# Kernel optimization log

Measured on AMD Instinct MI355X. Metric: run time of the kernel, lower is better.

Reference implementation:

```python
import jax, jax.numpy as jnp
import numpy as np
from jax import lax

S, B, VIN, VOUT, U, E = 64, 256, 128, 128, 1024, 512
START_CODE = 0
T_DEC = 25  # MAX_DECODE_STEPS


def gru_step(x, h, Wih, Whh, bih, bhh):
    # PyTorch GRU cell, gate order r,z,n
    gi = x @ Wih.T + bih
    gh = h @ Whh.T + bhh
    ir, iz, inn = jnp.split(gi, 3, axis=-1)
    hr, hz, hn = jnp.split(gh, 3, axis=-1)
    r = jax.nn.sigmoid(ir + hr)
    z = jax.nn.sigmoid(iz + hz)
    n = jnp.tanh(inn + r * hn)
    return (1.0 - z) * n + z * h


def setup_inputs() -> dict:
    key = jax.random.key(0)
    ks = jax.random.split(key, 20)
    sc = 0.05
    inp = {
        'x': jax.random.normal(ks[0], (S, B, VIN), jnp.float32),
        'x_len': jnp.maximum(jnp.sort(jax.random.randint(ks[1], (B,), 0, S + 1)), 1),
        'enc_Wih': jax.random.normal(ks[2], (3 * U, VIN), jnp.float32) * sc,
        'enc_Whh': jax.random.normal(ks[3], (3 * U, U), jnp.float32) * sc,
        'enc_bih': jnp.zeros((3 * U,), jnp.float32),
        'enc_bhh': jnp.zeros((3 * U,), jnp.float32),
        'dec_Wih': jax.random.normal(ks[4], (3 * U, E + U), jnp.float32) * sc,
        'dec_Whh': jax.random.normal(ks[5], (3 * U, U), jnp.float32) * sc,
        'dec_bih': jnp.zeros((3 * U,), jnp.float32),
        'dec_bhh': jnp.zeros((3 * U,), jnp.float32),
        'o2h_W': jax.random.normal(ks[6], (E, VOUT), jnp.float32) * sc,
        'o2h_b': jnp.zeros((E,), jnp.float32),
        'fc_W': jax.random.normal(ks[7], (VOUT, U), jnp.float32) * sc,
        'fc_b': jnp.zeros((VOUT,), jnp.float32),
        'W1_W': jax.random.normal(ks[8], (U, U), jnp.float32) * sc,
        'W1_b': jnp.zeros((U,), jnp.float32),
        'W2_W': jax.random.normal(ks[9], (U, U), jnp.float32) * sc,
        'W2_b': jnp.zeros((U,), jnp.float32),
        'V_W': jax.random.normal(ks[10], (1, U), jnp.float32) * sc,
        'V_b': jnp.zeros((1,), jnp.float32),
    }
    return inp


def _forward(x, x_len, enc_Wih, enc_Whh, enc_bih, enc_bhh,
             dec_Wih, dec_Whh, dec_bih, dec_bhh,
             o2h_W, o2h_b, fc_W, fc_b, W1_W, W1_b, W2_W, W2_b, V_W, V_b):
    # ---- Encoder GRU with length masking (pack/pad semantics) ----
    h0 = jnp.zeros((B, U), jnp.float32)
    t_idx = jnp.arange(S)

    def enc_step(h, inp_t):
        xt, t = inp_t
        mask = (t < x_len)[:, None]  # [B,1]
        hn = gru_step(xt, h, enc_Wih, enc_Whh, enc_bih, enc_bhh)
        h = jnp.where(mask, hn, h)
        out = jnp.where(mask, hn, 0.0)
        return h, out

    enc_hidden, enc_out = lax.scan(enc_step, h0, (x, t_idx))  # enc_out [S,B,U]
    enc_out = jnp.transpose(enc_out, (1, 0, 2))  # [B,S,U]

    # ---- Greedy decode (teacher_force=False), 25 steps ----
    enc_proj = enc_out @ W1_W.T + W1_b  # precompute W1(enc_output), [B,S,U]
    start = jnp.zeros((B, VOUT), jnp.float32).at[:, START_CODE].set(1.0)

    def dec_step(carry, _):
        h, dec_in = carry
        score = jnp.tanh(enc_proj + (h @ W2_W.T + W2_b)[:, None, :])  # [B,S,U]
        logits = score @ V_W.T + V_b  # [B,S,1]
        attn = jax.nn.softmax(logits, axis=1)
        ctx = jnp.sum(attn * enc_out, axis=1)  # [B,U]
        emb = dec_in @ o2h_W.T + o2h_b  # [B,E]
        gx = jnp.concatenate([ctx, emb], axis=-1)
        hn = gru_step(gx, h, dec_Wih, dec_Whh, dec_bih, dec_bhh)
        pred = hn @ fc_W.T + fc_b  # [B,VOUT]
        onehot = jax.nn.one_hot(jnp.argmax(pred, axis=-1), VOUT, dtype=pred.dtype)
        return (hn, lax.stop_gradient(onehot)), pred

    _, preds = lax.scan(dec_step, (enc_hidden, start), None, length=T_DEC - 1)
    return jnp.concatenate([start[None], preds], axis=0)  # [25,B,VOUT]


def reference(x, x_len, enc_Wih, enc_Whh, enc_bih, enc_bhh,
              dec_Wih, dec_Whh, dec_bih, dec_bhh,
              o2h_W, o2h_b, fc_W, fc_b, W1_W, W1_b, W2_W, W2_b, V_W, V_b):
    return _forward(x, x_len, enc_Wih, enc_Whh, enc_bih, enc_bhh,
                    dec_Wih, dec_Whh, dec_bih, dec_bhh,
                    o2h_W, o2h_b, fc_W, fc_b, W1_W, W1_b, W2_W, W2_b, V_W, V_b)
```

## Files before the change

### kernel.cpp

```cpp
#include <hip/hip_runtime.h>
#include <math.h>

#define SLEN 64
#define BATCH 256
#define VIND 128
#define VOUTD 128
#define UDIM 1024
#define EDIM 512
#define TDEC 25
#define GXW 1536
#define U3 3072
#define NSEG 12

typedef __attribute__((ext_vector_type(8))) short short8;
typedef __attribute__((ext_vector_type(4))) float f32x4;

#define MFMA(acc, A, B) acc = __builtin_amdgcn_mfma_f32_16x16x32_bf16((A), (B), (acc), 0, 0, 0)

__device__ __forceinline__ float sigm(float x) { return 1.f / (1.f + expf(-x)); }

__device__ __forceinline__ float tanhf_fast(float x) {
    float ax = fabsf(x);
    float e = __expf(-2.f * ax);
    float t = (1.f - e) / (1.f + e);
    return copysignf(t, x);
}

__device__ __forceinline__ short f2bf(float f) {
    unsigned u = __float_as_uint(f);
    u += 0x7FFF + ((u >> 16) & 1);
    return (short)(u >> 16);
}
__device__ __forceinline__ float bf2f(short h) {
    return __uint_as_float(((unsigned)(unsigned short)h) << 16);
}

__device__ __forceinline__ size_t pkChunk(int r, int k, int K) {
    return ((size_t)(r >> 4) * (K >> 5) + (k >> 5)) * 64 + ((r & 15) + 16 * ((k >> 3) & 3));
}

union S8 { short s[8]; short8 v; };

__device__ __forceinline__ void writeSplit8(short* Hi, short* Lo, size_t chunk,
                                            const float* vals) {
    S8 h, l;
#pragma unroll
    for (int j = 0; j < 8; j++) {
        short hb = f2bf(vals[j]);
        h.s[j] = hb;
        l.s[j] = f2bf(vals[j] - bf2f(hb));
    }
    ((short8*)Hi)[chunk] = h.v;
    ((short8*)Lo)[chunk] = l.v;
}

__global__ void init_kernel(float* __restrict__ h0, short* __restrict__ hpHi,
                            short* __restrict__ hpLo, float* __restrict__ out0,
                            int* __restrict__ idx,
                            const float* __restrict__ o2h_W,
                            const float* __restrict__ o2h_b,
                            float* __restrict__ o2hT) {
    int i = blockIdx.x * 256 + threadIdx.x;
    if (i < BATCH * UDIM) { h0[i] = 0.f; hpHi[i] = 0; hpLo[i] = 0; }
    if (i < BATCH * VOUTD) out0[i] = ((i & (VOUTD - 1)) == 0) ? 1.f : 0.f;
    if (i < BATCH) idx[i] = 0;
    if (i < VOUTD * EDIM) {
        int v = i >> 9, e = i & (EDIM - 1);
        o2hT[i] = o2h_W[(size_t)e * VOUTD + v] + o2h_b[e];
    }
}

struct PackSeg {
    const float* sA; const float* sB;
    short* Hi; short* Lo;
    int KA, KB, offA, offB, chunkStart;
};
struct PackArgs { PackSeg s[NSEG]; };

__global__ void pack_all(PackArgs pa, int total) {
    int gid = blockIdx.x * 256 + threadIdx.x;
    if (gid >= total) return;
    int si = 0;
#pragma unroll
    for (int i = 1; i < NSEG; i++) si = (gid >= pa.s[i].chunkStart) ? i : si;
    PackSeg sg = pa.s[si];
    int local = gid - sg.chunkStart;
    int K = sg.KA + sg.KB;
    int cpr = K >> 3;
    int r = local / cpr, k0 = (local - r * cpr) * 8;
    const float* src = (k0 < sg.KA)
        ? sg.sA + (size_t)(sg.offA + r) * sg.KA + k0
        : sg.sB + (size_t)(sg.offB + r) * sg.KB + (k0 - sg.KA);
    float v[8];
#pragma unroll
    for (int j = 0; j < 8; j++) v[j] = src[j];
    writeSplit8(sg.Hi, sg.Lo, pkChunk(r, k0, K), v);
}

__global__ __launch_bounds__(256) void gemm_w(
    const short8* __restrict__ Ahi, const short8* __restrict__ Alo,
    const short8* __restrict__ Whi, const short8* __restrict__ Wlo,
    const float* __restrict__ bias, float* __restrict__ C,
    int KT, int N) {
    int tid = threadIdx.x, lane = tid & 63, wave = tid >> 6;
    int m16 = blockIdx.x * 4 + (wave & 1) * 2;
    int nb = blockIdx.y * 8 + (wave >> 1) * 4;
    const short8* a0h = Ahi + (size_t)m16 * KT * 64 + lane;
    const short8* a1h = a0h + (size_t)KT * 64;
    const short8* a0l = Alo + (size_t)m16 * KT * 64 + lane;
    const short8* a1l = a0l + (size_t)KT * 64;
    const short8* w0h = Whi + (size_t)(nb + 0) * KT * 64 + lane;
    const short8* w1h = Whi + (size_t)(nb + 1) * KT * 64 + lane;
    const short8* w2h = Whi + (size_t)(nb + 2) * KT * 64 + lane;
    const short8* w3h = Whi + (size_t)(nb + 3) * KT * 64 + lane;
    const short8* w0l = Wlo + (size_t)(nb + 0) * KT * 64 + lane;
    const short8* w1l = Wlo + (size_t)(nb + 1) * KT * 64 + lane;
    const short8* w2l = Wlo + (size_t)(nb + 2) * KT * 64 + lane;
    const short8* w3l = Wlo + (size_t)(nb + 3) * KT * 64 + lane;
    f32x4 acc0[4] = {}, acc1[4] = {};

    for (int kt = 0; kt < KT; kt++) {
        size_t o = (size_t)kt * 64;
        short8 A0H = a0h[o], A1H = a1h[o], A0L = a0l[o], A1L = a1l[o];
        short8 WH0 = w0h[o], WL0 = w0l[o];
        MFMA(acc0[0], A0H, WH0); MFMA(acc1[0], A1H, WH0);
        MFMA(acc0[0], A0H, WL0); MFMA(acc1[0], A1H, WL0);
        MFMA(acc0[0], A0L, WH0); MFMA(acc1[0], A1L, WH0);
        short8 WH1 = w1h[o], WL1 = w1l[o];
        MFMA(acc0[1], A0H, WH1); MFMA(acc1[1], A1H, WH1);
        MFMA(acc0[1], A0H, WL1); MFMA(acc1[1], A1H, WL1);
        MFMA(acc0[1], A0L, WH1); MFMA(acc1[1], A1L, WH1);
        short8 WH2 = w2h[o], WL2 = w2l[o];
        MFMA(acc0[2], A0H, WH2); MFMA(acc1[2], A1H, WH2);
        MFMA(acc0[2], A0H, WL2); MFMA(acc1[2], A1H, WL2);
        MFMA(acc0[2], A0L, WH2); MFMA(acc1[2], A1L, WH2);
        short8 WH3 = w3h[o], WL3 = w3l[o];
        MFMA(acc0[3], A0H, WH3); MFMA(acc1[3], A1H, WH3);
        MFMA(acc0[3], A0H, WL3); MFMA(acc1[3], A1H, WL3);
        MFMA(acc0[3], A0L, WH3); MFMA(acc1[3], A1L, WH3);
    }
    int rsub = (lane >> 4) * 4, cn = lane & 15;
    int row0 = (m16 + 0) * 16 + rsub;
    int row1 = (m16 + 1) * 16 + rsub;
#pragma unroll
    for (int j = 0; j < 4; j++) {
        int col = (nb + j) * 16 + cn;
        float bb = bias ? bias[col] : 0.f;
#pragma unroll
        for (int r = 0; r < 4; r++) {
            C[(size_t)(row0 + r) * N + col] = acc0[j][r] + bb;
            C[(size_t)(row1 + r) * N + col] = acc1[j][r] + bb;
        }
    }
}

__global__ __launch_bounds__(256) void gemm_bm32(
    const short8* __restrict__ Ahi, const short8* __restrict__ Alo,
    const short8* __restrict__ Whi, const short8* __restrict__ Wlo,
    const float* __restrict__ bias, float* __restrict__ C,
    int KT, int N) {
    int tid = threadIdx.x, lane = tid & 63, wave = tid >> 6;
    int m16 = blockIdx.x * 2 + (wave & 1);
    int n16 = blockIdx.y * 4 + (wave >> 1) * 2;
    const short8* ah = Ahi + (size_t)m16 * KT * 64 + lane;
    const short8* al = Alo + (size_t)m16 * KT * 64 + lane;
    const short8* w0h = Whi + (size_t)n16 * KT * 64 + lane;
    const short8* w1h = w0h + (size_t)KT * 64;
    const short8* w0l = Wlo + (size_t)n16 * KT * 64 + lane;
    const short8* w1l = w0l + (size_t)KT * 64;
    f32x4 a0 = {0,0,0,0}, a1 = {0,0,0,0};
    for (int kt = 0; kt < KT; kt++) {
        size_t o = (size_t)kt * 64;
        short8 AH = ah[o], AL = al[o];
        short8 W0H = w0h[o], W0L = w0l[o], W1H = w1h[o], W1L = w1l[o];
        MFMA(a0, AH, W0H); MFMA(a1, AH, W1H);
        MFMA(a0, AH, W0L); MFMA(a1, AH, W1L);
        MFMA(a0, AL, W0H); MFMA(a1, AL, W1H);
    }
    int rsub = (lane >> 4) * 4, cn = lane & 15;
    float b0 = bias ? bias[(n16 + 0) * 16 + cn] : 0.f;
    float b1 = bias ? bias[(n16 + 1) * 16 + cn] : 0.f;
#pragma unroll
    for (int r = 0; r < 4; r++) {
        int row = m16 * 16 + rsub + r;
        C[(size_t)row * N + (n16 + 0) * 16 + cn] = a0[r] + b0;
        C[(size_t)row * N + (n16 + 1) * 16 + cn] = a1[r] + b1;
    }
}

__global__ __launch_bounds__(384) void enc_gru3(
    const short8* __restrict__ hinH8, const short8* __restrict__ hinL8,
    const short8* __restrict__ WrH, const short8* __restrict__ WrL,
    const short8* __restrict__ WzH, const short8* __restrict__ WzL,
    const short8* __restrict__ WnH, const short8* __restrict__ WnL,
    const float* __restrict__ gi,
    const float* __restrict__ bih, const float* __restrict__ bhh,
    const float* __restrict__ hinF, float* __restrict__ houtF,
    short* __restrict__ hoH, short* __restrict__ hoL,
    short* __restrict__ eaHi, short* __restrict__ eaLo,
    const int* __restrict__ x_len, int t) {
    __shared__ float sC[6][16][16];
    __shared__ float sHo[16][16];
    __shared__ float sEo[16][16];
    int tid = threadIdx.x, lane = tid & 63, wave = tid >> 6;
    int g = blockIdx.x;
    int m16 = blockIdx.y;
    int gate = wave >> 1, half = wave & 1;
    const short8* ah = hinH8 + (size_t)m16 * 32 * 64 + (size_t)half * 16 * 64 + lane;
    const short8* al = hinL8 + (size_t)m16 * 32 * 64 + (size_t)half * 16 * 64 + lane;
    const short8* WH0 = (gate == 0) ? WrH : (gate == 1) ? WzH : WnH;
    const short8* WL0 = (gate == 0) ? WrL : (gate == 1) ? WzL : WnL;
    const short8* wh = WH0 + (size_t)g * 32 * 64 + (size_t)half * 16 * 64 + lane;
    const short8* wl = WL0 + (size_t)g * 32 * 64 + (size_t)half * 16 * 64 + lane;
    f32x4 acc = {0, 0, 0, 0};
    for (int kt = 0; kt < 16; kt++) {
        size_t o = (size_t)kt * 64;
        short8 AH = ah[o], AL = al[o];
        short8 WH = wh[o], WL = wl[o];
        MFMA(acc, AH, WH);
        MFMA(acc, AH, WL);
        MFMA(acc, AL, WH);
    }
    {
        int rsub = (lane >> 4) << 2, cn = lane & 15;
#pragma unroll
        for (int j = 0; j < 4; j++) sC[wave][rsub + j][cn] = acc[j];
    }
    __syncthreads();
    if (wave == 0) {
        int cu = g * 16 + (lane & 15);
        int rsub = (lane >> 4) << 2;
        float b_r = bih[cu] + bhh[cu];
        float b_z = bih[UDIM + cu] + bhh[UDIM + cu];
        float b_nh = bhh[2 * UDIM + cu];
        float b_ni = bih[2 * UDIM + cu];
        int growLocal = (t & 7) * 256;
#pragma unroll
        for (int j = 0; j < 4; j++) {
            int rr = rsub + j, cc = lane & 15;
            int b = m16 * 16 + rr;
            const float* gr = gi + (size_t)(growLocal + b) * U3;
            float rg = sigm(sC[0][rr][cc] + sC[1][rr][cc] + gr[cu] + b_r);
            float zg = sigm(sC[2][rr][cc] + sC[3][rr][cc] + gr[UDIM + cu] + b_z);
            float nn = tanhf(gr[2 * UDIM + cu] + b_ni +
                             rg * (sC[4][rr][cc] + sC[5][rr][cc] + b_nh));
            float hp = hinF[(size_t)b * UDIM + cu];
            float hv = (1.f - zg) * nn + zg * hp;
            bool msk = t < x_len[b];
            float ho = msk ? hv : hp;
            houtF[(size_t)b * UDIM + cu] = ho;
            sHo[rr][cc] = ho;
            sEo[rr][cc] = msk ? hv : 0.f;
        }
    }
    __syncthreads();
    if (wave == 1 && lane < 32) {
        int rr = lane >> 1, oct = lane & 1;
        int brow = m16 * 16 + rr;
        int u0 = g * 16 + oct * 8;
        float v[8];
#pragma unroll
        for (int j = 0; j < 8; j++) v[j] = sHo[rr][oct * 8 + j];
        writeSplit8(hoH, hoL, pkChunk(brow, u0, UDIM), v);
#pragma unroll
        for (int j = 0; j < 8; j++) v[j] = sEo[rr][oct * 8 + j];
        writeSplit8(eaHi, eaLo, pkChunk(brow * SLEN + t, u0, UDIM), v);
    }
}

__global__ __launch_bounds__(384) void dec_gru3(
    const short8* __restrict__ hinH8, const short8* __restrict__ hinL8,
    const short8* __restrict__ gxH8, const short8* __restrict__ gxL8,
    const short8* __restrict__ WrH, const short8* __restrict__ WrL,
    const short8* __restrict__ WzH, const short8* __restrict__ WzL,
    const short8* __restrict__ WnhH, const short8* __restrict__ WnhL,
    const short8* __restrict__ WniH, const short8* __restrict__ WniL,
    const float* __restrict__ bih, const float* __restrict__ bhh,
    const float* __restrict__ hinF, float* __restrict__ houtF,
    short* __restrict__ hoH, short* __restrict__ hoL) {
    __shared__ float sC[8][16][16];
    __shared__ float sHo[16][16];
    int tid = threadIdx.x, lane = tid & 63, wave = tid >> 6;
    int g = blockIdx.x;
    int m16 = blockIdx.y;
    int gate = wave >> 1, half = wave & 1;
    const short8* ah = hinH8 + (size_t)m16 * 32 * 64 + (size_t)half * 16 * 64 + lane;
    const short8* al = hinL8 + (size_t)m16 * 32 * 64 + (size_t)half * 16 * 64 + lane;
    const short8* gxh = gxH8 + (size_t)m16 * 48 * 64 + (size_t)half * 24 * 64 + lane;
    const short8* gxl = gxL8 + (size_t)m16 * 48 * 64 + (size_t)half * 24 * 64 + lane;
    const short8 *whA, *wlA, *whB, *wlB;
    if (gate == 0) {
        whA = WrH + (size_t)g * 80 * 64 + (size_t)half * 16 * 64 + lane;
        wlA = WrL + (size_t)g * 80 * 64 + (size_t)half * 16 * 64 + lane;
        whB = WrH + (size_t)g * 80 * 64 + (size_t)(32 + half * 24) * 64 + lane;
        wlB = WrL + (size_t)g * 80 * 64 + (size_t)(32 + half * 24) * 64 + lane;
    } else if (gate == 1) {
        whA = WzH + (size_t)g * 80 * 64 + (size_t)half * 16 * 64 + lane;
        wlA = WzL + (size_t)g * 80 * 64 + (size_t)half * 16 * 64 + lane;
        whB = WzH + (size_t)g * 80 * 64 + (size_t)(32 + half * 24) * 64 + lane;
        wlB = WzL + (size_t)g * 80 * 64 + (size_t)(32 + half * 24) * 64 + lane;
    } else {
        whA = WnhH + (size_t)g * 32 * 64 + (size_t)half * 16 * 64 + lane;
        wlA = WnhL + (size_t)g * 32 * 64 + (size_t)half * 16 * 64 + lane;
        whB = WniH + (size_t)g * 48 * 64 + (size_t)half * 24 * 64 + lane;
        wlB = WniL + (size_t)g * 48 * 64 + (size_t)half * 24 * 64 + lane;
    }
    f32x4 accA = {0,0,0,0}, accB = {0,0,0,0};
    for (int kt = 0; kt < 16; kt++) {
        size_t o = (size_t)kt * 64;
        short8 AH = ah[o], AL = al[o];
        short8 WH = whA[o], WL = wlA[o];
        MFMA(accA, AH, WH);
        MFMA(accA, AH, WL);
        MFMA(accA, AL, WH);
    }
    for (int kt = 0; kt < 24; kt++) {
        size_t o = (size_t)kt * 64;
        short8 AH = gxh[o], AL = gxl[o];
        short8 WH = whB[o], WL = wlB[o];
        MFMA(accB, AH, WH);
        MFMA(accB, AH, WL);
        MFMA(accB, AL, WH);
    }
    {
        int rsub = (lane >> 4) << 2, cn = lane & 15;
        if (wave < 4) {
#pragma unroll
            for (int j = 0; j < 4; j++) sC[wave][rsub + j][cn] = accA[j] + accB[j];
        } else {
#pragma unroll
            for (int j = 0; j < 4; j++) {
                sC[wave][rsub + j][cn] = accA[j];
                sC[wave + 2][rsub + j][cn] = accB[j];
            }
        }
    }
    __syncthreads();
    if (wave == 0) {
        int cu = g * 16 + (lane & 15);
        int rsub = (lane >> 4) << 2;
        float b_r = bih[cu] + bhh[cu];
        float b_z = bih[UDIM + cu] + bhh[UDIM + cu];
        float b_nh = bhh[2 * UDIM + cu];
        float b_ni = bih[2 * UDIM + cu];
#pragma unroll
        for (int j = 0; j < 4; j++) {
            int rr = rsub + j, cc = lane & 15;
            int b = m16 * 16 + rr;
            float rg = sigm(sC[0][rr][cc] + sC[1][rr][cc] + b_r);
            float zg = sigm(sC[2][rr][cc] + sC[3][rr][cc] + b_z);
            float nn = tanhf(sC[6][rr][cc] + sC[7][rr][cc] + b_ni +
                             rg * (sC[4][rr][cc] + sC[5][rr][cc] + b_nh));
            float hp = hinF[(size_t)b * UDIM + cu];
            float hv = (1.f - zg) * nn + zg * hp;
            houtF[(size_t)b * UDIM + cu] = hv;
            sHo[rr][cc] = hv;
        }
    }
    __syncthreads();
    if (wave == 1 && lane < 32) {
        int rr = lane >> 1, oct = lane & 1;
        int brow = m16 * 16 + rr;
        int u0 = g * 16 + oct * 8;
        float v[8];
#pragma unroll
        for (int j = 0; j < 8; j++) v[j] = sHo[rr][oct * 8 + j];
        writeSplit8(hoH, hoL, pkChunk(brow, u0, UDIM), v);
    }
}

__global__ __launch_bounds__(1024) void attn_ctx(
    const float* __restrict__ encProj,
    const short* __restrict__ eaHi, const short* __restrict__ eaLo,
    const float* __restrict__ tmp2, const float* __restrict__ V_W,
    const float* __restrict__ V_b,
    const float* __restrict__ o2hT,
    const int* __restrict__ idx, short* __restrict__ gxHi, short* __restrict__ gxLo) {
    int b = blockIdx.x;
    int tid = threadIdx.x, lane = tid & 63, wave = tid >> 6;
    __shared__ float s_t2[UDIM];
    __shared__ float s_v[UDIM];
    __shared__ float s_attn[SLEN];
    __shared__ float s_part[7][128][9];
    for (int u = tid; u < UDIM; u += 1024) {
        s_t2[u] = tmp2[(size_t)b * UDIM + u];
        s_v[u] = V_W[u];
    }
    __syncthreads();
    for (int s = wave; s < SLEN; s += 16) {
        const float4* ep4 = (const float4*)(encProj + ((size_t)b * SLEN + s) * UDIM);
        float p = 0.f;
        for (int u4 = lane; u4 < UDIM / 4; u4 += 64) {
            float4 e = ep4[u4];
            int u = 4 * u4;
            p += tanhf_fast(e.x + s_t2[u]) * s_v[u] +
                 tanhf_fast(e.y + s_t2[u + 1]) * s_v[u + 1] +
                 tanhf_fast(e.z + s_t2[u + 2]) * s_v[u + 2] +
                 tanhf_fast(e.w + s_t2[u + 3]) * s_v[u + 3];
        }
#pragma unroll
        for (int off = 32; off > 0; off >>= 1) p += __shfl_xor(p, off);
        if (lane == 0) s_attn[s] = p + V_b[0];
    }
    __syncthreads();
    if (tid < 64) {
        float v = s_attn[tid];
        float mx = v;
#pragma unroll
        for (int off = 32; off > 0; off >>= 1) mx = fmaxf(mx, __shfl_xor(mx, off));
        float e = expf(v - mx);
        float sum = e;
#pragma unroll
        for (int off = 32; off > 0; off >>= 1) sum += __shfl_xor(sum, off);
        s_attn[tid] = e / sum;
    }
    __syncthreads();
    {
        int grp = tid >> 7, tu = tid & 127;
        int u0 = tu * 8;
        float a[8] = {0, 0, 0, 0, 0, 0, 0, 0};
        const short8* hi8 = (const short8*)eaHi;
        const short8* lo8 = (const short8*)eaLo;
        int lanePart = 16 * ((u0 >> 3) & 3);
        int colPart = u0 >> 5;
        for (int s = grp * 8; s < grp * 8 + 8; s++) {
            int r = b * SLEN + s;
            size_t ch = ((size_t)(r >> 4) * (UDIM >> 5) + colPart) * 64 + (r & 15) + lanePart;
            S8 h, l;
            h.v = hi8[ch];
            l.v = lo8[ch];
            float w = s_attn[s];
#pragma unroll
            for (int j = 0; j < 8; j++) a[j] += w * (bf2f(h.s[j]) + bf2f(l.s[j]));
        }
        if (grp) {
#pragma unroll
            for (int j = 0; j < 8; j++) s_part[grp - 1][tu][j] = a[j];
        }
        __syncthreads();
        if (tid < 128) {
#pragma unroll
            for (int gg = 0; gg < 7; gg++)
#pragma unroll
                for (int j = 0; j < 8; j++) a[j] += s_part[gg][tu][j];
            writeSplit8(gxHi, gxLo, pkChunk(b, u0, GXW), a);
        } else if (tid < 192) {
            int e0 = (tid - 128) * 8;
            int ib = idx[b];
            const float* row = o2hT + (size_t)ib * EDIM + e0;
            float v[8];
#pragma unroll
            for (int j = 0; j < 8; j++) v[j] = row[j];
            writeSplit8(gxHi, gxLo, pkChunk(b, UDIM + e0, GXW), v);
        }
    }
}

__global__ __launch_bounds__(256) void fcw2(
    const short8* __restrict__ hHi, const short8* __restrict__ hLo,
    const short8* __restrict__ fcH, const short8* __restrict__ fcL,
    const float* __restrict__ fc_b, float* __restrict__ pred,
    int* __restrict__ idx,
    const short8* __restrict__ w2H, const short8* __restrict__ w2L,
    const float* __restrict__ W2_b, float* __restrict__ tmp2) {
    __shared__ float sP[16][129];
    int tid = threadIdx.x, lane = tid & 63, wave = tid >> 6;
    if (blockIdx.x < 16) {
        int fm = blockIdx.x;
        const short8* ah = hHi + (size_t)fm * 32 * 64 + lane;
        const short8* al = hLo + (size_t)fm * 32 * 64 + lane;
        int n0 = 2 * wave, n1 = 2 * wave + 1;
        const short8* w0h = fcH + (size_t)n0 * 32 * 64 + lane;
        const short8* w0l = fcL + (size_t)n0 * 32 * 64 + lane;
        const short8* w1h = fcH + (size_t)n1 * 32 * 64 + lane;
        const short8* w1l = fcL + (size_t)n1 * 32 * 64 + lane;
        f32x4 a0 = {0,0,0,0}, a1 = {0,0,0,0};
        for (int kt = 0; kt < 32; kt++) {
            size_t o = (size_t)kt * 64;
            short8 AH = ah[o], AL = al[o];
            short8 W0H = w0h[o], W0L = w0l[o], W1H = w1h[o], W1L = w1l[o];
            MFMA(a0, AH, W0H); MFMA(a1, AH, W1H);
            MFMA(a0, AH, W0L); MFMA(a1, AH, W1L);
            MFMA(a0, AL, W0H); MFMA(a1, AL, W1H);
        }
        int cn = lane & 15, rsub = (lane >> 4) << 2;
#pragma unroll
        for (int j = 0; j < 4; j++) {
            sP[rsub + j][n0 * 16 + cn] = a0[j] + fc_b[n0 * 16 + cn];
            sP[rsub + j][n1 * 16 + cn] = a1[j] + fc_b[n1 * 16 + cn];
        }
        __syncthreads();
        {
            int row = tid >> 4, c0 = (tid & 15) * 8;
            float* pr = pred + (size_t)(fm * 16 + row) * VOUTD;
#pragma unroll
            for (int j = 0; j < 8; j++) pr[c0 + j] = sP[row][c0 + j];
        }
        if (tid < 128) {
            int row = tid >> 3, seg = tid & 7;
            float v = -1e30f;
            int bi = 0;
            int c0 = seg * 16;
            for (int j = c0; j < c0 + 16; j++) {
                float w = sP[row][j];
                if (w > v) { v = w; bi = j; }
            }
#pragma unroll
            for (int off = 1; off < 8; off <<= 1) {
                float ov = __shfl_xor(v, off);
                int obi = __shfl_xor(bi, off);
                if (ov > v || (ov == v && obi < bi)) { v = ov; bi = obi; }
            }
            if (seg == 0) idx[fm * 16 + row] = bi;
        }
    } else {
        int lin = blockIdx.x - 16;
        int bx = lin & 7, by = lin >> 3;
        int m16 = bx * 2 + (wave & 1);
        int n16 = by * 4 + (wave >> 1) * 2;
        const short8* ah = hHi + (size_t)m16 * 32 * 64 + lane;
        const short8* al = hLo + (size_t)m16 * 32 * 64 + lane;
        const short8* w0h = w2H + (size_t)n16 * 32 * 64 + lane;
        const short8* w1h = w0h + (size_t)32 * 64;
        const short8* w0l = w2L + (size_t)n16 * 32 * 64 + lane;
        const short8* w1l = w0l + (size_t)32 * 64;
        f32x4 a0 = {0,0,0,0}, a1 = {0,0,0,0};
        for (int kt = 0; kt < 32; kt++) {
            size_t o = (size_t)kt * 64;
            short8 AH = ah[o], AL = al[o];
            short8 W0H = w0h[o], W0L = w0l[o], W1H = w1h[o], W1L = w1l[o];
            MFMA(a0, AH, W0H); MFMA(a1, AH, W1H);
            MFMA(a0, AH, W0L); MFMA(a1, AH, W1L);
            MFMA(a0, AL, W0H); MFMA(a1, AL, W1H);
        }
        int rsub = (lane >> 4) * 4, cn = lane & 15;
        float b0 = W2_b[(n16 + 0) * 16 + cn];
        float b1 = W2_b[(n16 + 1) * 16 + cn];
#pragma unroll
        for (int r = 0; r < 4; r++) {
            int row = m16 * 16 + rsub + r;
            tmp2[(size_t)row * UDIM + (n16 + 0) * 16 + cn] = a0[r] + b0;
            tmp2[(size_t)row * UDIM + (n16 + 1) * 16 + cn] = a1[r] + b1;
        }
    }
}

extern "C" void kernel_launch(void* const* d_in, const int* in_sizes, int n_in,
                              void* d_out, int out_size, void* d_ws, size_t ws_size,
                              hipStream_t stream) {
    const float* x       = (const float*)d_in[0];
    const int*   x_len   = (const int*)d_in[1];
    const float* enc_Wih = (const float*)d_in[2];
    const float* enc_Whh = (const float*)d_in[3];
    const float* enc_bih = (const float*)d_in[4];
    const float* enc_bhh = (const float*)d_in[5];
    const float* dec_Wih = (const float*)d_in[6];
    const float* dec_Whh = (const float*)d_in[7];
    const float* dec_bih = (const float*)d_in[8];
    const float* dec_bhh = (const float*)d_in[9];
    const float* o2h_W   = (const float*)d_in[10];
    const float* o2h_b   = (const float*)d_in[11];
    const float* fc_W    = (const float*)d_in[12];
    const float* fc_b    = (const float*)d_in[13];
    const float* W1_W    = (const float*)d_in[14];
    const float* W1_b    = (const float*)d_in[15];
    const float* W2_W    = (const float*)d_in[16];
    const float* W2_b    = (const float*)d_in[17];
    const float* V_W     = (const float*)d_in[18];
    const float* V_b     = (const float*)d_in[19];
    float* out = (float*)d_out;

    char* p = (char*)d_ws;
    auto alloc = [&](size_t bytes) -> char* {
        char* q = p;
        p += (bytes + 255) & ~(size_t)255;
        return q;
    };
    float* hAF  = (float*)alloc((size_t)BATCH * UDIM * 4);
    float* hBF  = (float*)alloc((size_t)BATCH * UDIM * 4);
    short* hAH  = (short*)alloc((size_t)BATCH * UDIM * 2);
    short* hAL  = (short*)alloc((size_t)BATCH * UDIM * 2);
    short* hBH  = (short*)alloc((size_t)BATCH * UDIM * 2);
    short* hBL  = (short*)alloc((size_t)BATCH * UDIM * 2);
    float* tmp2 = (float*)alloc((size_t)BATCH * UDIM * 4);
    short* gxHi = (short*)alloc((size_t)BATCH * GXW * 2);
    short* gxLo = (short*)alloc((size_t)BATCH * GXW * 2);
    short* encAHi = (short*)alloc((size_t)BATCH * SLEN * UDIM * 2);
    short* encALo = (short*)alloc((size_t)BATCH * SLEN * UDIM * 2);
    float* encProjF = (float*)alloc((size_t)BATCH * SLEN * UDIM * 4);
    float* gihBuf = (float*)alloc((size_t)8 * BATCH * U3 * 4);
    short* eWihH = (short*)alloc((size_t)U3 * VIND * 2);
    short* eWihL = (short*)alloc((size_t)U3 * VIND * 2);
    short* eWrH = (short*)alloc((size_t)UDIM * UDIM * 2);
    short* eWrL = (short*)alloc((size_t)UDIM * UDIM * 2);
    short* eWzH = (short*)alloc((size_t)UDIM * UDIM * 2);
    short* eWzL = (short*)alloc((size_t)UDIM * UDIM * 2);
    short* eWnH = (short*)alloc((size_t)UDIM * UDIM * 2);
    short* eWnL = (short*)alloc((size_t)UDIM * UDIM * 2);
    short* dWrH = (short*)alloc((size_t)UDIM * 2560 * 2);
    short* dWrL = (short*)alloc((size_t)UDIM * 2560 * 2);
    short* dWzH = (short*)alloc((size_t)UDIM * 2560 * 2);
    short* dWzL = (short*)alloc((size_t)UDIM * 2560 * 2);
    short* dWnhH = (short*)alloc((size_t)UDIM * UDIM * 2);
    short* dWnhL = (short*)alloc((size_t)UDIM * UDIM * 2);
    short* dWniH = (short*)alloc((size_t)UDIM * GXW * 2);
    short* dWniL = (short*)alloc((size_t)UDIM * GXW * 2);
    short* w1Hi = (short*)alloc((size_t)UDIM * UDIM * 2);
    short* w1Lo = (short*)alloc((size_t)UDIM * UDIM * 2);
    short* w2Hi = (short*)alloc((size_t)UDIM * UDIM * 2);
    short* w2Lo = (short*)alloc((size_t)UDIM * UDIM * 2);
    short* fcHi = (short*)alloc((size_t)VOUTD * UDIM * 2);
    short* fcLo = (short*)alloc((size_t)VOUTD * UDIM * 2);
    short* xHi  = (short*)alloc((size_t)SLEN * BATCH * VIND * 2);
    short* xLo  = (short*)alloc((size_t)SLEN * BATCH * VIND * 2);
    int*   idx  = (int*)alloc(BATCH * 4);
    float* o2hT = (float*)alloc((size_t)VOUTD * EDIM * 4);

    init_kernel<<<(BATCH * UDIM + 255) / 256, 256, 0, stream>>>(
        hAF, hAH, hAL, out, idx, o2h_W, o2h_b, o2hT);

    {
        PackArgs pa;
        int cs = 0, n = 0;
        auto seg = [&](const float* sA, int KA, int offA, const float* sB, int KB,
                       int offB, short* Hi, short* Lo, int R) {
            pa.s[n] = {sA, sB, Hi, Lo, KA, KB, offA, offB, cs};
            cs += R * (KA + KB) / 8;
            n++;
        };
        seg(enc_Wih, VIND, 0, nullptr, 0, 0, eWihH, eWihL, U3);
        seg(enc_Whh, UDIM, 0, nullptr, 0, 0, eWrH, eWrL, UDIM);
        seg(enc_Whh, UDIM, UDIM, nullptr, 0, 0, eWzH, eWzL, UDIM);
        seg(enc_Whh, UDIM, 2 * UDIM, nullptr, 0, 0, eWnH, eWnL, UDIM);
        seg(dec_Whh, UDIM, 0, dec_Wih, GXW, 0, dWrH, dWrL, UDIM);
        seg(dec_Whh, UDIM, UDIM, dec_Wih, GXW, UDIM, dWzH, dWzL, UDIM);
        seg(dec_Whh, UDIM, 2 * UDIM, nullptr, 0, 0, dWnhH, dWnhL, UDIM);
        seg(dec_Wih, GXW, 2 * UDIM, nullptr, 0, 0, dWniH, dWniL, UDIM);
        seg(W1_W, UDIM, 0, nullptr, 0, 0, w1Hi, w1Lo, UDIM);
        seg(W2_W, UDIM, 0, nullptr, 0, 0, w2Hi, w2Lo, UDIM);
        seg(fc_W, UDIM, 0, nullptr, 0, 0, fcHi, fcLo, VOUTD);
        seg(x, VIND, 0, nullptr, 0, 0, xHi, xLo, SLEN * BATCH);
        pack_all<<<(cs + 255) / 256, 256, 0, stream>>>(pa, cs);
    }

    float* hcF = hAF; float* hnF = hBF;
    short *hcH = hAH, *hcL = hAL, *hnH = hBH, *hnL = hBL;
    for (int c = 0; c < 8; c++) {
        gemm_w<<<dim3(32, 24), 256, 0, stream>>>(
            (const short8*)xHi + (size_t)c * 128 * 4 * 64,
            (const short8*)xLo + (size_t)c * 128 * 4 * 64,
            (const short8*)eWihH, (const short8*)eWihL,
            nullptr, gihBuf, VIND / 32, U3);
        for (int tt = 0; tt < 8; tt++) {
            int t = c * 8 + tt;
            enc_gru3<<<dim3(64, 16), 384, 0, stream>>>(
                (const short8*)hcH, (const short8*)hcL,
                (const short8*)eWrH, (const short8*)eWrL,
                (const short8*)eWzH, (const short8*)eWzL,
                (const short8*)eWnH, (const short8*)eWnL,
                gihBuf, enc_bih, enc_bhh, hcF, hnF, hnH, hnL,
                encAHi, encALo, x_len, t);
            { float* tf = hcF; hcF = hnF; hnF = tf; }
            { short* th = hcH; hcH = hnH; hnH = th; th = hcL; hcL = hnL; hnL = th; }
        }
    }

    gemm_w<<<dim3(SLEN * BATCH / 64, UDIM / 128), 256, 0, stream>>>(
        (const short8*)encAHi, (const short8*)encALo,
        (const short8*)w1Hi, (const short8*)w1Lo,
        W1_b, encProjF, UDIM / 32, UDIM);

    gemm_bm32<<<dim3(BATCH / 32, UDIM / 64), 256, 0, stream>>>(
        (const short8*)hcH, (const short8*)hcL,
        (const short8*)w2Hi, (const short8*)w2Lo,
        W2_b, tmp2, UDIM / 32, UDIM);

    for (int st = 0; st < TDEC - 1; st++) {
        attn_ctx<<<BATCH, 1024, 0, stream>>>(
            encProjF, encAHi, encALo, tmp2, V_W, V_b, o2hT, idx, gxHi, gxLo);
        dec_gru3<<<dim3(64, 16), 384, 0, stream>>>(
            (const short8*)hcH, (const short8*)hcL,
            (const short8*)gxHi, (const short8*)gxLo,
            (const short8*)dWrH, (const short8*)dWrL,
            (const short8*)dWzH, (const short8*)dWzL,
            (const short8*)dWnhH, (const short8*)dWnhL,
            (const short8*)dWniH, (const short8*)dWniL,
            dec_bih, dec_bhh, hcF, hnF, hnH, hnL);
        float* pred = out + (size_t)(1 + st) * BATCH * VOUTD;
        fcw2<<<144, 256, 0, stream>>>(
            (const short8*)hnH, (const short8*)hnL,
            (const short8*)fcHi, (const short8*)fcLo,
            fc_b, pred, idx,
            (const short8*)w2Hi, (const short8*)w2Lo, W2_b, tmp2);
        { float* tf = hcF; hcF = hnF; hnF = tf; }
        { short* th = hcH; hcH = hnH; hnH = th; th = hcL; hcL = hnL; hnL = th; }
    }
}
```

Baseline: 4.143 ms.

## Split fused GRU step kernels into tiled gate GEMM plus elementwise tail

Replaces the fused per-step encoder and decoder GRU kernels with two launches per step. The first is a generic 32-row tiled MFMA GEMM that writes all gate pre-activations to a global buffer; the second is an elementwise tail kernel that applies the gate nonlinearities. The decoder hidden state is now packed together with ctx and emb into one concatenated K=2560 input, so a single GEMM covers all four gate regions, and this buffer is double-buffered. The aim is better weight reuse and occupancy in the GEMM, at the cost of extra launches and a global round trip for the gate values.

```diff
diff --git a/kernel.cpp b/kernel.cpp
--- a/kernel.cpp
+++ b/kernel.cpp
@@ -8,9 +8,9 @@
 #define UDIM 1024
 #define EDIM 512
 #define TDEC 25
-#define GXW 1536
 #define U3 3072
-#define NSEG 12
+#define DECK 2560
+#define NSEG 10
 
 typedef __attribute__((ext_vector_type(8))) short short8;
 typedef __attribute__((ext_vector_type(4))) float f32x4;
@@ -188,185 +188,105 @@
     }
 }
 
-__global__ __launch_bounds__(384) void enc_gru3(
-    const short8* __restrict__ hinH8, const short8* __restrict__ hinL8,
+__global__ __launch_bounds__(256) void gemm_dec(
+    const short8* __restrict__ Ahi, const short8* __restrict__ Alo,
     const short8* __restrict__ WrH, const short8* __restrict__ WrL,
     const short8* __restrict__ WzH, const short8* __restrict__ WzL,
-    const short8* __restrict__ WnH, const short8* __restrict__ WnL,
+    const short8* __restrict__ WnhH, const short8* __restrict__ WnhL,
+    const short8* __restrict__ WniH, const short8* __restrict__ WniL,
+    float* __restrict__ gh) {
+    int tid = threadIdx.x, lane = tid & 63, wave = tid >> 6;
+    int m16 = blockIdx.x * 2 + (wave & 1);
+    int by = blockIdx.y;
+    int reg = by >> 4;
+    int KT = (reg < 2) ? 80 : (reg == 2 ? 32 : 48);
+    int aoff = (reg == 3) ? 32 : 0;
+    const short8 *BH, *BL;
+    if (reg == 0) { BH = WrH; BL = WrL; }
+    else if (reg == 1) { BH = WzH; BL = WzL; }
+    else if (reg == 2) { BH = WnhH; BL = WnhL; }
+    else { BH = WniH; BL = WniL; }
+    int nloc = (by & 15) * 4 + (wave >> 1) * 2;
+    const short8* ah = Ahi + (size_t)m16 * 80 * 64 + (size_t)aoff * 64 + lane;
+    const short8* al = Alo + (size_t)m16 * 80 * 64 + (size_t)aoff * 64 + lane;
+    const short8* w0h = BH + (size_t)nloc * KT * 64 + lane;
+    const short8* w1h = w0h + (size_t)KT * 64;
+    const short8* w0l = BL + (size_t)nloc * KT * 64 + lane;
+    const short8* w1l = w0l + (size_t)KT * 64;
+    f32x4 a0 = {0,0,0,0}, a1 = {0,0,0,0};
+    for (int kt = 0; kt < KT; kt++) {
+        size_t o = (size_t)kt * 64;
+        short8 AH = ah[o], AL = al[o];
+        short8 W0H = w0h[o], W0L = w0l[o], W1H = w1h[o], W1L = w1l[o];
+        MFMA(a0, AH, W0H); MFMA(a1, AH, W1H);
+        MFMA(a0, AH, W0L); MFMA(a1, AH, W1L);
+        MFMA(a0, AL, W0H); MFMA(a1, AL, W1H);
+    }
+    int rsub = (lane >> 4) * 4, cn = lane & 15;
+    int c0 = (reg * 64 + nloc) * 16 + cn;
+#pragma unroll
+    for (int r = 0; r < 4; r++) {
+        int row = m16 * 16 + rsub + r;
+        gh[(size_t)row * 4096 + c0] = a0[r];
+        gh[(size_t)row * 4096 + c0 + 16] = a1[r];
+    }
+}
+
+__global__ __launch_bounds__(256) void enc_tail(
+    const float* __restrict__ gh,
     const float* __restrict__ gi,
     const float* __restrict__ bih, const float* __restrict__ bhh,
     const float* __restrict__ hinF, float* __restrict__ houtF,
     short* __restrict__ hoH, short* __restrict__ hoL,
     short* __restrict__ eaHi, short* __restrict__ eaLo,
+    short* __restrict__ hgxH, short* __restrict__ hgxL,
     const int* __restrict__ x_len, int t) {
-    __shared__ float sC[6][16][16];
-    __shared__ float sHo[16][16];
-    __shared__ float sEo[16][16];
-    int tid = threadIdx.x, lane = tid & 63, wave = tid >> 6;
-    int g = blockIdx.x;
-    int m16 = blockIdx.y;
-    int gate = wave >> 1, half = wave & 1;
-    const short8* ah = hinH8 + (size_t)m16 * 32 * 64 + (size_t)half * 16 * 64 + lane;
-    const short8* al = hinL8 + (size_t)m16 * 32 * 64 + (size_t)half * 16 * 64 + lane;
-    const short8* WH0 = (gate == 0) ? WrH : (gate == 1) ? WzH : WnH;
-    const short8* WL0 = (gate == 0) ? WrL : (gate == 1) ? WzL : WnL;
-    const short8* wh = WH0 + (size_t)g * 32 * 64 + (size_t)half * 16 * 64 + lane;
-    const short8* wl = WL0 + (size_t)g * 32 * 64 + (size_t)half * 16 * 64 + lane;
-    f32x4 acc = {0, 0, 0, 0};
-    for (int kt = 0; kt < 16; kt++) {
-        size_t o = (size_t)kt * 64;
-        short8 AH = ah[o], AL = al[o];
-        short8 WH = wh[o], WL = wl[o];
-        MFMA(acc, AH, WH);
-        MFMA(acc, AH, WL);
-        MFMA(acc, AL, WH);
-    }
-    {
-        int rsub = (lane >> 4) << 2, cn = lane & 15;
-#pragma unroll
-        for (int j = 0; j < 4; j++) sC[wave][rsub + j][cn] = acc[j];
-    }
-    __syncthreads();
-    if (wave == 0) {
-        int cu = g * 16 + (lane & 15);
-        int rsub = (lane >> 4) << 2;
-        float b_r = bih[cu] + bhh[cu];
-        float b_z = bih[UDIM + cu] + bhh[UDIM + cu];
-        float b_nh = bhh[2 * UDIM + cu];
-        float b_ni = bih[2 * UDIM + cu];
-        int growLocal = (t & 7) * 256;
-#pragma unroll
-        for (int j = 0; j < 4; j++) {
-            int rr = rsub + j, cc = lane & 15;
-            int b = m16 * 16 + rr;
-            const float* gr = gi + (size_t)(growLocal + b) * U3;
-            float rg = sigm(sC[0][rr][cc] + sC[1][rr][cc] + gr[cu] + b_r);
-            float zg = sigm(sC[2][rr][cc] + sC[3][rr][cc] + gr[UDIM + cu] + b_z);
-            float nn = tanhf(gr[2 * UDIM + cu] + b_ni +
-                             rg * (sC[4][rr][cc] + sC[5][rr][cc] + b_nh));
-            float hp = hinF[(size_t)b * UDIM + cu];
-            float hv = (1.f - zg) * nn + zg * hp;
-            bool msk = t < x_len[b];
-            float ho = msk ? hv : hp;
-            houtF[(size_t)b * UDIM + cu] = ho;
-            sHo[rr][cc] = ho;
-            sEo[rr][cc] = msk ? hv : 0.f;
-        }
-    }
-    __syncthreads();
-    if (wave == 1 && lane < 32) {
-        int rr = lane >> 1, oct = lane & 1;
-        int brow = m16 * 16 + rr;
-        int u0 = g * 16 + oct * 8;
-        float v[8];
-#pragma unroll
-        for (int j = 0; j < 8; j++) v[j] = sHo[rr][oct * 8 + j];
-        writeSplit8(hoH, hoL, pkChunk(brow, u0, UDIM), v);
-#pragma unroll
-        for (int j = 0; j < 8; j++) v[j] = sEo[rr][oct * 8 + j];
-        writeSplit8(eaHi, eaLo, pkChunk(brow * SLEN + t, u0, UDIM), v);
-    }
-}
-
-__global__ __launch_bounds__(384) void dec_gru3(
-    const short8* __restrict__ hinH8, const short8* __restrict__ hinL8,
-    const short8* __restrict__ gxH8, const short8* __restrict__ gxL8,
-    const short8* __restrict__ WrH, const short8* __restrict__ WrL,
-    const short8* __restrict__ WzH, const short8* __restrict__ WzL,
-    const short8* __restrict__ WnhH, const short8* __restrict__ WnhL,
-    const short8* __restrict__ WniH, const short8* __restrict__ WniL,
+    int row = blockIdx.x * 2 + (threadIdx.x >> 7);
+    int u0 = (threadIdx.x & 127) * 8;
+    const float* g = gh + (size_t)row * U3;
+    const float* gr = gi + (size_t)((t & 7) * 256 + row) * U3;
+    bool msk = t < x_len[row];
+    float ho[8], eo[8];
+#pragma unroll
+    for (int j = 0; j < 8; j++) {
+        int u = u0 + j;
+        float rg = sigm(g[u] + gr[u] + bih[u] + bhh[u]);
+        float zg = sigm(g[UDIM + u] + gr[UDIM + u] + bih[UDIM + u] + bhh[UDIM + u]);
+        float nn = tanhf(gr[2 * UDIM + u] + bih[2 * UDIM + u] +
+                         rg * (g[2 * UDIM + u] + bhh[2 * UDIM + u]));
+        float hp = hinF[(size_t)row * UDIM + u];
+        float hv = (1.f - zg) * nn + zg * hp;
+        ho[j] = msk ? hv : hp;
+        eo[j] = msk ? hv : 0.f;
+        houtF[(size_t)row * UDIM + u] = ho[j];
+    }
+    writeSplit8(hoH, hoL, pkChunk(row, u0, UDIM), ho);
+    writeSplit8(eaHi, eaLo, pkChunk(row * SLEN + t, u0, UDIM), eo);
+    if (hgxH) writeSplit8(hgxH, hgxL, pkChunk(row, u0, DECK), ho);
+}
+
+__global__ __launch_bounds__(256) void dec_tail(
+    const float* __restrict__ gh,
     const float* __restrict__ bih, const float* __restrict__ bhh,
     const float* __restrict__ hinF, float* __restrict__ houtF,
-    short* __restrict__ hoH, short* __restrict__ hoL) {
-    __shared__ float sC[8][16][16];
-    __shared__ float sHo[16][16];
-    int tid = threadIdx.x, lane = tid & 63, wave = tid >> 6;
-    int g = blockIdx.x;
-    int m16 = blockIdx.y;
-    int gate = wave >> 1, half = wave & 1;
-    const short8* ah = hinH8 + (size_t)m16 * 32 * 64 + (size_t)half * 16 * 64 + lane;
-    const short8* al = hinL8 + (size_t)m16 * 32 * 64 + (size_t)half * 16 * 64 + lane;
-    const short8* gxh = gxH8 + (size_t)m16 * 48 * 64 + (size_t)half * 24 * 64 + lane;
-    const short8* gxl = gxL8 + (size_t)m16 * 48 * 64 + (size_t)half * 24 * 64 + lane;
-    const short8 *whA, *wlA, *whB, *wlB;
-    if (gate == 0) {
-        whA = WrH + (size_t)g * 80 * 64 + (size_t)half * 16 * 64 + lane;
-        wlA = WrL + (size_t)g * 80 * 64 + (size_t)half * 16 * 64 + lane;
-        whB = WrH + (size_t)g * 80 * 64 + (size_t)(32 + half * 24) * 64 + lane;
-        wlB = WrL + (size_t)g * 80 * 64 + (size_t)(32 + half * 24) * 64 + lane;
-    } else if (gate == 1) {
-        whA = WzH + (size_t)g * 80 * 64 + (size_t)half * 16 * 64 + lane;
-        wlA = WzL + (size_t)g * 80 * 64 + (size_t)half * 16 * 64 + lane;
-        whB = WzH + (size_t)g * 80 * 64 + (size_t)(32 + half * 24) * 64 + lane;
-        wlB = WzL + (size_t)g * 80 * 64 + (size_t)(32 + half * 24) * 64 + lane;
-    } else {
-        whA = WnhH + (size_t)g * 32 * 64 + (size_t)half * 16 * 64 + lane;
-        wlA = WnhL + (size_t)g * 32 * 64 + (size_t)half * 16 * 64 + lane;
-        whB = WniH + (size_t)g * 48 * 64 + (size_t)half * 24 * 64 + lane;
-        wlB = WniL + (size_t)g * 48 * 64 + (size_t)half * 24 * 64 + lane;
-    }
-    f32x4 accA = {0,0,0,0}, accB = {0,0,0,0};
-    for (int kt = 0; kt < 16; kt++) {
-        size_t o = (size_t)kt * 64;
-        short8 AH = ah[o], AL = al[o];
-        short8 WH = whA[o], WL = wlA[o];
-        MFMA(accA, AH, WH);
-        MFMA(accA, AH, WL);
-        MFMA(accA, AL, WH);
-    }
-    for (int kt = 0; kt < 24; kt++) {
-        size_t o = (size_t)kt * 64;
-        short8 AH = gxh[o], AL = gxl[o];
-        short8 WH = whB[o], WL = wlB[o];
-        MFMA(accB, AH, WH);
-        MFMA(accB, AH, WL);
-        MFMA(accB, AL, WH);
-    }
-    {
-        int rsub = (lane >> 4) << 2, cn = lane & 15;
-        if (wave < 4) {
-#pragma unroll
-            for (int j = 0; j < 4; j++) sC[wave][rsub + j][cn] = accA[j] + accB[j];
-        } else {
-#pragma unroll
-            for (int j = 0; j < 4; j++) {
-                sC[wave][rsub + j][cn] = accA[j];
-                sC[wave + 2][rsub + j][cn] = accB[j];
-            }
-        }
-    }
-    __syncthreads();
-    if (wave == 0) {
-        int cu = g * 16 + (lane & 15);
-        int rsub = (lane >> 4) << 2;
-        float b_r = bih[cu] + bhh[cu];
-        float b_z = bih[UDIM + cu] + bhh[UDIM + cu];
-        float b_nh = bhh[2 * UDIM + cu];
-        float b_ni = bih[2 * UDIM + cu];
-#pragma unroll
-        for (int j = 0; j < 4; j++) {
-            int rr = rsub + j, cc = lane & 15;
-            int b = m16 * 16 + rr;
-            float rg = sigm(sC[0][rr][cc] + sC[1][rr][cc] + b_r);
-            float zg = sigm(sC[2][rr][cc] + sC[3][rr][cc] + b_z);
-            float nn = tanhf(sC[6][rr][cc] + sC[7][rr][cc] + b_ni +
-                             rg * (sC[4][rr][cc] + sC[5][rr][cc] + b_nh));
-            float hp = hinF[(size_t)b * UDIM + cu];
-            float hv = (1.f - zg) * nn + zg * hp;
-            houtF[(size_t)b * UDIM + cu] = hv;
-            sHo[rr][cc] = hv;
-        }
-    }
-    __syncthreads();
-    if (wave == 1 && lane < 32) {
-        int rr = lane >> 1, oct = lane & 1;
-        int brow = m16 * 16 + rr;
-        int u0 = g * 16 + oct * 8;
-        float v[8];
-#pragma unroll
-        for (int j = 0; j < 8; j++) v[j] = sHo[rr][oct * 8 + j];
-        writeSplit8(hoH, hoL, pkChunk(brow, u0, UDIM), v);
-    }
+    short* __restrict__ hgxH, short* __restrict__ hgxL) {
+    int row = blockIdx.x * 2 + (threadIdx.x >> 7);
+    int u0 = (threadIdx.x & 127) * 8;
+    const float* g = gh + (size_t)row * 4096;
+    float ho[8];
+#pragma unroll
+    for (int j = 0; j < 8; j++) {
+        int u = u0 + j;
+        float rg = sigm(g[u] + bih[u] + bhh[u]);
+        float zg = sigm(g[1024 + u] + bih[UDIM + u] + bhh[UDIM + u]);
+        float nn = tanhf(g[3072 + u] + bih[2 * UDIM + u] +
+                         rg * (g[2048 + u] + bhh[2 * UDIM + u]));
+        float hp = hinF[(size_t)row * UDIM + u];
+        float hv = (1.f - zg) * nn + zg * hp;
+        ho[j] = hv;
+        houtF[(size_t)row * UDIM + u] = hv;
+    }
+    writeSplit8(hgxH, hgxL, pkChunk(row, u0, DECK), ho);
 }
 
 __global__ __launch_bounds__(1024) void attn_ctx(
@@ -429,9 +349,9 @@
             S8 h, l;
             h.v = hi8[ch];
             l.v = lo8[ch];
-            float w = s_attn[s];
-#pragma unroll
-            for (int j = 0; j < 8; j++) a[j] += w * (bf2f(h.s[j]) + bf2f(l.s[j]));
+            float wt = s_attn[s];
+#pragma unroll
+            for (int j = 0; j < 8; j++) a[j] += wt * (bf2f(h.s[j]) + bf2f(l.s[j]));
         }
         if (grp) {
 #pragma unroll
@@ -443,7 +363,7 @@
             for (int gg = 0; gg < 7; gg++)
 #pragma unroll
                 for (int j = 0; j < 8; j++) a[j] += s_part[gg][tu][j];
-            writeSplit8(gxHi, gxLo, pkChunk(b, u0, GXW), a);
+            writeSplit8(gxHi, gxLo, pkChunk(b, 1024 + u0, DECK), a);
         } else if (tid < 192) {
             int e0 = (tid - 128) * 8;
             int ib = idx[b];
@@ -451,7 +371,7 @@
             float v[8];
 #pragma unroll
             for (int j = 0; j < 8; j++) v[j] = row[j];
-            writeSplit8(gxHi, gxLo, pkChunk(b, UDIM + e0, GXW), v);
+            writeSplit8(gxHi, gxLo, pkChunk(b, 2048 + e0, DECK), v);
         }
     }
 }
@@ -467,8 +387,8 @@
     int tid = threadIdx.x, lane = tid & 63, wave = tid >> 6;
     if (blockIdx.x < 16) {
         int fm = blockIdx.x;
-        const short8* ah = hHi + (size_t)fm * 32 * 64 + lane;
-        const short8* al = hLo + (size_t)fm * 32 * 64 + lane;
+        const short8* ah = hHi + (size_t)fm * 80 * 64 + lane;
+        const short8* al = hLo + (size_t)fm * 80 * 64 + lane;
         int n0 = 2 * wave, n1 = 2 * wave + 1;
         const short8* w0h = fcH + (size_t)n0 * 32 * 64 + lane;
         const short8* w0l = fcL + (size_t)n0 * 32 * 64 + lane;
@@ -518,8 +438,8 @@
         int bx = lin & 7, by = lin >> 3;
         int m16 = bx * 2 + (wave & 1);
         int n16 = by * 4 + (wave >> 1) * 2;
-        const short8* ah = hHi + (size_t)m16 * 32 * 64 + lane;
-        const short8* al = hLo + (size_t)m16 * 32 * 64 + lane;
+        const short8* ah = hHi + (size_t)m16 * 80 * 64 + lane;
+        const short8* al = hLo + (size_t)m16 * 80 * 64 + lane;
         const short8* w0h = w2H + (size_t)n16 * 32 * 64 + lane;
         const short8* w1h = w0h + (size_t)32 * 64;
         const short8* w0l = w2L + (size_t)n16 * 32 * 64 + lane;
@@ -583,28 +503,28 @@
     short* hBH  = (short*)alloc((size_t)BATCH * UDIM * 2);
     short* hBL  = (short*)alloc((size_t)BATCH * UDIM * 2);
     float* tmp2 = (float*)alloc((size_t)BATCH * UDIM * 4);
-    short* gxHi = (short*)alloc((size_t)BATCH * GXW * 2);
-    short* gxLo = (short*)alloc((size_t)BATCH * GXW * 2);
+    short* hgxAH = (short*)alloc((size_t)BATCH * DECK * 2);
+    short* hgxAL = (short*)alloc((size_t)BATCH * DECK * 2);
+    short* hgxBH = (short*)alloc((size_t)BATCH * DECK * 2);
+    short* hgxBL = (short*)alloc((size_t)BATCH * DECK * 2);
+    float* ghEnc = (float*)alloc((size_t)BATCH * U3 * 4);
+    float* ghDec = (float*)alloc((size_t)BATCH * 4096 * 4);
     short* encAHi = (short*)alloc((size_t)BATCH * SLEN * UDIM * 2);
     short* encALo = (short*)alloc((size_t)BATCH * SLEN * UDIM * 2);
     float* encProjF = (float*)alloc((size_t)BATCH * SLEN * UDIM * 4);
     float* gihBuf = (float*)alloc((size_t)8 * BATCH * U3 * 4);
     short* eWihH = (short*)alloc((size_t)U3 * VIND * 2);
     short* eWihL = (short*)alloc((size_t)U3 * VIND * 2);
-    short* eWrH = (short*)alloc((size_t)UDIM * UDIM * 2);
-    short* eWrL = (short*)alloc((size_t)UDIM * UDIM * 2);
-    short* eWzH = (short*)alloc((size_t)UDIM * UDIM * 2);
-    short* eWzL = (short*)alloc((size_t)UDIM * UDIM * 2);
-    short* eWnH = (short*)alloc((size_t)UDIM * UDIM * 2);
-    short* eWnL = (short*)alloc((size_t)UDIM * UDIM * 2);
-    short* dWrH = (short*)alloc((size_t)UDIM * 2560 * 2);
-    short* dWrL = (short*)alloc((size_t)UDIM * 2560 * 2);
-    short* dWzH = (short*)alloc((size_t)UDIM * 2560 * 2);
-    short* dWzL = (short*)alloc((size_t)UDIM * 2560 * 2);
+    short* eWhhH = (short*)alloc((size_t)U3 * UDIM * 2);
+    short* eWhhL = (short*)alloc((size_t)U3 * UDIM * 2);
+    short* dWrH = (short*)alloc((size_t)UDIM * DECK * 2);
+    short* dWrL = (short*)alloc((size_t)UDIM * DECK * 2);
+    short* dWzH = (short*)alloc((size_t)UDIM * DECK * 2);
+    short* dWzL = (short*)alloc((size_t)UDIM * DECK * 2);
     short* dWnhH = (short*)alloc((size_t)UDIM * UDIM * 2);
     short* dWnhL = (short*)alloc((size_t)UDIM * UDIM * 2);
-    short* dWniH = (short*)alloc((size_t)UDIM * GXW * 2);
-    short* dWniL = (short*)alloc((size_t)UDIM * GXW * 2);
+    short* dWniH = (short*)alloc((size_t)UDIM * 1536 * 2);
+    short* dWniL = (short*)alloc((size_t)UDIM * 1536 * 2);
     short* w1Hi = (short*)alloc((size_t)UDIM * UDIM * 2);
     short* w1Lo = (short*)alloc((size_t)UDIM * UDIM * 2);
     short* w2Hi = (short*)alloc((size_t)UDIM * UDIM * 2);
@@ -629,13 +549,11 @@
             n++;
         };
         seg(enc_Wih, VIND, 0, nullptr, 0, 0, eWihH, eWihL, U3);
-        seg(enc_Whh, UDIM, 0, nullptr, 0, 0, eWrH, eWrL, UDIM);
-        seg(enc_Whh, UDIM, UDIM, nullptr, 0, 0, eWzH, eWzL, UDIM);
-        seg(enc_Whh, UDIM, 2 * UDIM, nullptr, 0, 0, eWnH, eWnL, UDIM);
-        seg(dec_Whh, UDIM, 0, dec_Wih, GXW, 0, dWrH, dWrL, UDIM);
-        seg(dec_Whh, UDIM, UDIM, dec_Wih, GXW, UDIM, dWzH, dWzL, UDIM);
+        seg(enc_Whh, UDIM, 0, nullptr, 0, 0, eWhhH, eWhhL, U3);
+        seg(dec_Whh, UDIM, 0, dec_Wih, 1536, 0, dWrH, dWrL, UDIM);
+        seg(dec_Whh, UDIM, UDIM, dec_Wih, 1536, UDIM, dWzH, dWzL, UDIM);
         seg(dec_Whh, UDIM, 2 * UDIM, nullptr, 0, 0, dWnhH, dWnhL, UDIM);
-        seg(dec_Wih, GXW, 2 * UDIM, nullptr, 0, 0, dWniH, dWniL, UDIM);
+        seg(dec_Wih, 1536, 2 * UDIM, nullptr, 0, 0, dWniH, dWniL, UDIM);
         seg(W1_W, UDIM, 0, nullptr, 0, 0, w1Hi, w1Lo, UDIM);
         seg(W2_W, UDIM, 0, nullptr, 0, 0, w2Hi, w2Lo, UDIM);
         seg(fc_W, UDIM, 0, nullptr, 0, 0, fcHi, fcLo, VOUTD);
@@ -653,13 +571,16 @@
             nullptr, gihBuf, VIND / 32, U3);
         for (int tt = 0; tt < 8; tt++) {
             int t = c * 8 + tt;
-            enc_gru3<<<dim3(64, 16), 384, 0, stream>>>(
+            gemm_bm32<<<dim3(8, 48), 256, 0, stream>>>(
                 (const short8*)hcH, (const short8*)hcL,
-                (const short8*)eWrH, (const short8*)eWrL,
-                (const short8*)eWzH, (const short8*)eWzL,
-                (const short8*)eWnH, (const short8*)eWnL,
-                gihBuf, enc_bih, enc_bhh, hcF, hnF, hnH, hnL,
-                encAHi, encALo, x_len, t);
+                (const short8*)eWhhH, (const short8*)eWhhL,
+                nullptr, ghEnc, 32, U3);
+            enc_tail<<<128, 256, 0, stream>>>(
+                ghEnc, gihBuf, enc_bih, enc_bhh, hcF, hnF, hnH, hnL,
+                encAHi, encALo,
+                (t == SLEN - 1) ? hgxAH : (short*)nullptr,
+                (t == SLEN - 1) ? hgxAL : (short*)nullptr,
+                x_len, t);
             { float* tf = hcF; hcF = hnF; hnF = tf; }
             { short* th = hcH; hcH = hnH; hnH = th; th = hcL; hcL = hnL; hnL = th; }
         }
@@ -675,24 +596,27 @@
         (const short8*)w2Hi, (const short8*)w2Lo,
         W2_b, tmp2, UDIM / 32, UDIM);
 
+    short* hgH[2] = {hgxAH, hgxBH};
+    short* hgL[2] = {hgxAL, hgxBL};
     for (int st = 0; st < TDEC - 1; st++) {
+        int cur = st & 1, nxt = cur ^ 1;
         attn_ctx<<<BATCH, 1024, 0, stream>>>(
-            encProjF, encAHi, encALo, tmp2, V_W, V_b, o2hT, idx, gxHi, gxLo);
-        dec_gru3<<<dim3(64, 16), 384, 0, stream>>>(
-            (const short8*)hcH, (const short8*)hcL,
-            (const short8*)gxHi, (const short8*)gxLo,
+            encProjF, encAHi, encALo, tmp2, V_W, V_b, o2hT, idx,
+            hgH[cur], hgL[cur]);
+        gemm_dec<<<dim3(8, 64), 256, 0, stream>>>(
+            (const short8*)hgH[cur], (const short8*)hgL[cur],
             (const short8*)dWrH, (const short8*)dWrL,
             (const short8*)dWzH, (const short8*)dWzL,
             (const short8*)dWnhH, (const short8*)dWnhL,
-            (const short8*)dWniH, (const short8*)dWniL,
-            dec_bih, dec_bhh, hcF, hnF, hnH, hnL);
+            (const short8*)dWniH, (const short8*)dWniL, ghDec);
+        dec_tail<<<128, 256, 0, stream>>>(
+            ghDec, dec_bih, dec_bhh, hcF, hnF, hgH[nxt], hgL[nxt]);
         float* pred = out + (size_t)(1 + st) * BATCH * VOUTD;
         fcw2<<<144, 256, 0, stream>>>(
-            (const short8*)hnH, (const short8*)hnL,
+            (const short8*)hgH[nxt], (const short8*)hgL[nxt],
             (const short8*)fcHi, (const short8*)fcLo,
             fc_b, pred, idx,
             (const short8*)w2Hi, (const short8*)w2Lo, W2_b, tmp2);
         { float* tf = hcF; hcF = hnF; hnF = tf; }
-        { short* th = hcH; hcH = hnH; hnH = th; th = hcL; hcL = hnL; hnL = th; }
-    }
-}
+    }
+}
```

New measurement: 6.481 ms. 1.56x slower.
